# Performance work log

Measured on AMD Instinct MI355X. Metric: run time of the kernel, lower is better.

Reference implementation:

```python
import jax, jax.numpy as jnp
import numpy as np

IN, H, B = 1024, 1024, 8192
EPS = 1e-5

def _ln(x, g, b):
    mu = jnp.mean(x, axis=-1, keepdims=True)
    var = jnp.mean(jnp.square(x - mu), axis=-1, keepdims=True)
    return (x - mu) * jax.lax.rsqrt(var + EPS) * g + b

def setup_inputs() -> dict:
    key = jax.random.key(0)
    ks = jax.random.split(key, 6)
    inp = {
        "input": jax.random.normal(ks[0], (B, IN), dtype=jnp.float32),
        "h_prev": jax.random.normal(ks[1], (B, H), dtype=jnp.float32),
        "c_prev": jax.random.normal(ks[2], (B, H), dtype=jnp.float32),
        # Linear(in, 4H, bias=False) weights, stored [out, in] like torch
        "w_i": jax.random.normal(ks[3], (4 * H, IN), dtype=jnp.float32) / np.sqrt(IN),
        "w_h": jax.random.normal(ks[4], (4 * H, H), dtype=jnp.float32) / np.sqrt(H),
    }
    for name in ("ln_i", "ln_h", "ln_g", "ln_o", "ln_c"):
        inp[name + "_g"] = jnp.ones((H,), dtype=jnp.float32)
        inp[name + "_b"] = jnp.zeros((H,), dtype=jnp.float32)
    return inp

def reference(input, h_prev, c_prev, w_i, w_h,
              ln_i_g, ln_i_b, ln_h_g, ln_h_b, ln_g_g, ln_g_b,
              ln_o_g, ln_o_b, ln_c_g, ln_c_b):
    gi = input @ w_i.T            # [B, 4H]
    gh = h_prev @ w_h.T           # [B, 4H]
    i_i, i_f, i_gc, i_o = jnp.split(gi, 4, axis=-1)
    h_i, h_f, h_g, h_o = jnp.split(gh, 4, axis=-1)
    i_g = jax.nn.sigmoid(_ln(i_i + h_i, ln_i_g, ln_i_b))
    f_g = jax.nn.sigmoid(_ln(i_f + h_f, ln_h_g, ln_h_b))
    # NOTE: faithful to source bug — uses sigmoided i_g (not chunk i_gc) here
    g_g = jnp.tanh(_ln(i_g + h_g, ln_g_g, ln_g_b))
    o_g = jax.nn.sigmoid(_ln(i_o + h_o, ln_o_g, ln_o_b))
    c_new = _ln(f_g * c_prev + i_g * g_g, ln_c_g, ln_c_b)
    h_new = o_g * jnp.tanh(c_new)
    return (h_new, c_new)
```

## Files before the change

kernel.cpp:

```cpp
#include <hip/hip_runtime.h>
#include <hip/hip_bf16.h>

#define BATCH 8192
#define HDIM  1024
#define KDIM  2048
#define NDIM  4096

__device__ inline unsigned short f2bf(float x) {
    unsigned int u = __float_as_uint(x);
    unsigned int r = (u + 0x7fffu + ((u >> 16) & 1u)) >> 16;
    return (unsigned short)r;
}

__global__ __launch_bounds__(256) void convert_w_kernel(
    const float* __restrict__ wi, const float* __restrict__ wh,
    unsigned short* __restrict__ Wb)
{
    int idx = blockIdx.x * 256 + threadIdx.x;
    int n = idx >> 9;
    int k = (idx & 511) << 2;
    float4 v;
    if (k < 1024) {
        if (n >= 2048 && n < 3072) {
            v = make_float4(0.f, 0.f, 0.f, 0.f);
        } else {
            v = *(const float4*)(wi + (size_t)n * 1024 + k);
        }
    } else {
        v = *(const float4*)(wh + (size_t)n * 1024 + (k - 1024));
    }
    ushort4 o;
    o.x = f2bf(v.x); o.y = f2bf(v.y); o.z = f2bf(v.z); o.w = f2bf(v.w);
    *(ushort4*)(Wb + (size_t)n * KDIM + k) = o;
}

__global__ __launch_bounds__(256) void convert_x_kernel(
    const float* __restrict__ input, const float* __restrict__ h_prev,
    unsigned short* __restrict__ Xb)
{
    int idx = blockIdx.x * 256 + threadIdx.x;
    int r = idx >> 9;
    int k = (idx & 511) << 2;
    float4 v;
    if (k < 1024) {
        v = *(const float4*)(input + (size_t)r * 1024 + k);
    } else {
        v = *(const float4*)(h_prev + (size_t)r * 1024 + (k - 1024));
    }
    ushort4 o;
    o.x = f2bf(v.x); o.y = f2bf(v.y); o.z = f2bf(v.z); o.w = f2bf(v.w);
    *(ushort4*)(Xb + (size_t)r * KDIM + k) = o;
}

#define BM 256
#define BN 128
#define BK 64

typedef __attribute__((ext_vector_type(8))) short bf16x8;
typedef __attribute__((ext_vector_type(4))) float f32x4;

__global__ __launch_bounds__(512) void gemm_bt_kernel(
    const unsigned short* __restrict__ A,
    const unsigned short* __restrict__ Bw,
    float* __restrict__ C,
    int M)
{
    __shared__ unsigned short As[BM * BK];
    __shared__ unsigned short Bs[BN * BK];

    const int tid  = threadIdx.x;
    const int lane = tid & 63;
    const int wave = tid >> 6;

    const int bid = blockIdx.x;
    const int bm  = (bid >> 5) * BM;
    const int bn  = (bid & 31) * BN;

    f32x4 acc[4][4] = {};

    const int wm = (wave >> 1) * 64;
    const int wn = (wave & 1) * 64;

    const int srow = lane >> 3;
    const int c_sw = (lane & 7) ^ srow;

    int k0 = 0;
    if (bn >= 2048 && bn < 3072) k0 = 1024;

    for (; k0 < KDIM; k0 += BK) {
#pragma unroll
        for (int p = 0; p < 4; ++p) {
            const int rbase = wave * 32 + p * 8;
            const unsigned short* gA =
                A + (size_t)(bm + rbase + srow) * KDIM + k0 + c_sw * 8;
            __builtin_amdgcn_global_load_lds(
                (const __attribute__((address_space(1))) void*)gA,
                (__attribute__((address_space(3))) void*)&As[rbase * BK], 16, 0, 0);
        }
#pragma unroll
        for (int p = 0; p < 2; ++p) {
            const int rbase = wave * 16 + p * 8;
            const unsigned short* gB =
                Bw + (size_t)(bn + rbase + srow) * KDIM + k0 + c_sw * 8;
            __builtin_amdgcn_global_load_lds(
                (const __attribute__((address_space(1))) void*)gB,
                (__attribute__((address_space(3))) void*)&Bs[rbase * BK], 16, 0, 0);
        }
        __syncthreads();

#pragma unroll
        for (int kk = 0; kk < 2; ++kk) {
            bf16x8 af[4], bfr[4];
            const int cbase = kk * 4 + (lane >> 4);
#pragma unroll
            for (int i = 0; i < 4; ++i) {
                const int ra = wm + i * 16 + (lane & 15);
                af[i]  = *(const bf16x8*)&As[ra * BK + ((cbase ^ (ra & 7)) * 8)];
                const int rb = wn + i * 16 + (lane & 15);
                bfr[i] = *(const bf16x8*)&Bs[rb * BK + ((cbase ^ (rb & 7)) * 8)];
            }
#pragma unroll
            for (int i = 0; i < 4; ++i)
#pragma unroll
                for (int j = 0; j < 4; ++j)
                    acc[i][j] = __builtin_amdgcn_mfma_f32_16x16x32_bf16(
                        af[i], bfr[j], acc[i][j], 0, 0, 0);
        }
        __syncthreads();
    }

#pragma unroll
    for (int i = 0; i < 4; ++i) {
#pragma unroll
        for (int j = 0; j < 4; ++j) {
#pragma unroll
            for (int r = 0; r < 4; ++r) {
                int row = bm + wm + i * 16 + (lane >> 4) * 4 + r;
                int col = bn + wn + j * 16 + (lane & 15);
                C[(size_t)row * NDIM + col] = acc[i][j][r];
            }
        }
    }
}

__device__ inline float sigmoid_f(float x) { return 1.f / (1.f + __expf(-x)); }
__device__ inline float tanh_f(float x) { return 1.f - 2.f / (__expf(2.f * x) + 1.f); }

__device__ inline void wstats(const float* x, float& mu, float& rs)
{
    float s = 0.f, q = 0.f;
#pragma unroll
    for (int e = 0; e < 16; ++e) { s += x[e]; q += x[e] * x[e]; }
#pragma unroll
    for (int o = 1; o < 64; o <<= 1) {
        s += __shfl_xor(s, o);
        q += __shfl_xor(q, o);
    }
    mu = s * (1.f / 1024.f);
    float var = q * (1.f / 1024.f) - mu * mu;
    rs = rsqrtf(var + 1e-5f);
}

#define LOAD16(dst, base)                                              \
    _Pragma("unroll")                                                  \
    for (int j = 0; j < 4; ++j) {                                      \
        float4 t = *(const float4*)((base) + j * 256 + cbase);         \
        dst[4 * j] = t.x; dst[4 * j + 1] = t.y;                        \
        dst[4 * j + 2] = t.z; dst[4 * j + 3] = t.w;                    \
    }

__global__ __launch_bounds__(256) void lstm_ew_kernel(
    const float* __restrict__ G,
    const float* __restrict__ c_prev,
    const float* __restrict__ p0g, const float* __restrict__ p0b,
    const float* __restrict__ p1g, const float* __restrict__ p1b,
    const float* __restrict__ p2g, const float* __restrict__ p2b,
    const float* __restrict__ p3g, const float* __restrict__ p3b,
    const float* __restrict__ p4g, const float* __restrict__ p4b,
    float* __restrict__ out_h, float* __restrict__ out_c,
    int row_base)
{
    const int lane  = threadIdx.x & 63;
    const int wave  = threadIdx.x >> 6;
    const int r     = blockIdx.x * 4 + wave;
    const int grow  = row_base + r;
    const int cbase = lane * 4;

    const float* Grow = G + (size_t)r * NDIM;

    float tmp[16], pg[16], pb[16];
    float ig[16], cm[16], og[16];
    float mu, rs;

    LOAD16(tmp, Grow);
    wstats(tmp, mu, rs);
    LOAD16(pg, p0g); LOAD16(pb, p0b);
#pragma unroll
    for (int e = 0; e < 16; ++e)
        ig[e] = sigmoid_f((tmp[e] - mu) * rs * pg[e] + pb[e]);

    LOAD16(tmp, Grow + 1024);
    wstats(tmp, mu, rs);
    LOAD16(pg, p1g); LOAD16(pb, p1b);
    LOAD16(cm, c_prev + (size_t)grow * HDIM);
#pragma unroll
    for (int e = 0; e < 16; ++e)
        cm[e] *= sigmoid_f((tmp[e] - mu) * rs * pg[e] + pb[e]);

    LOAD16(tmp, Grow + 2048);
#pragma unroll
    for (int e = 0; e < 16; ++e) tmp[e] += ig[e];
    wstats(tmp, mu, rs);
    LOAD16(pg, p2g); LOAD16(pb, p2b);
#pragma unroll
    for (int e = 0; e < 16; ++e)
        cm[e] += ig[e] * tanh_f((tmp[e] - mu) * rs * pg[e] + pb[e]);

    LOAD16(tmp, Grow + 3072);
    wstats(tmp, mu, rs);
    LOAD16(pg, p3g); LOAD16(pb, p3b);
#pragma unroll
    for (int e = 0; e < 16; ++e)
        og[e] = sigmoid_f((tmp[e] - mu) * rs * pg[e] + pb[e]);

    wstats(cm, mu, rs);
    LOAD16(pg, p4g); LOAD16(pb, p4b);
    float cn[16], hn[16];
#pragma unroll
    for (int e = 0; e < 16; ++e) {
        cn[e] = (cm[e] - mu) * rs * pg[e] + pb[e];
        hn[e] = og[e] * tanh_f(cn[e]);
    }

    float* oh = out_h + (size_t)grow * HDIM;
    float* oc = out_c + (size_t)grow * HDIM;
#pragma unroll
    for (int j = 0; j < 4; ++j) {
        *(float4*)(oh + j * 256 + cbase) =
            make_float4(hn[4 * j], hn[4 * j + 1], hn[4 * j + 2], hn[4 * j + 3]);
        *(float4*)(oc + j * 256 + cbase) =
            make_float4(cn[4 * j], cn[4 * j + 1], cn[4 * j + 2], cn[4 * j + 3]);
    }
}

extern "C" void kernel_launch(void* const* d_in, const int* in_sizes, int n_in,
                              void* d_out, int out_size, void* d_ws, size_t ws_size,
                              hipStream_t stream)
{
    const float* input  = (const float*)d_in[0];
    const float* h_prev = (const float*)d_in[1];
    const float* c_prev = (const float*)d_in[2];
    const float* w_i    = (const float*)d_in[3];
    const float* w_h    = (const float*)d_in[4];
    const float* lng[10];
    for (int i = 0; i < 10; ++i) lng[i] = (const float*)d_in[5 + i];

    unsigned short* Xb = (unsigned short*)d_ws;
    size_t xb_bytes = (size_t)BATCH * KDIM * 2;
    unsigned short* Wb = (unsigned short*)((char*)d_ws + xb_bytes);
    size_t wb_bytes = (size_t)NDIM * KDIM * 2;
    float* G = (float*)((char*)d_ws + xb_bytes + wb_bytes);

    size_t g_avail = (ws_size > xb_bytes + wb_bytes) ? (ws_size - xb_bytes - wb_bytes) : 0;
    long max_rows = (long)(g_avail / ((size_t)NDIM * sizeof(float)));
    int chunk = (max_rows >= BATCH) ? BATCH : (int)((max_rows / BM) * BM);
    if (chunk <= 0) chunk = BM;

    convert_w_kernel<<<(NDIM * 512) / 256, 256, 0, stream>>>(w_i, w_h, Wb);
    convert_x_kernel<<<(BATCH * 512) / 256, 256, 0, stream>>>(input, h_prev, Xb);

    float* out_h = (float*)d_out;
    float* out_c = out_h + (size_t)BATCH * HDIM;

    for (int rb = 0; rb < BATCH; rb += chunk) {
        int rows = (BATCH - rb < chunk) ? (BATCH - rb) : chunk;
        gemm_bt_kernel<<<(rows / BM) * (NDIM / BN), 512, 0, stream>>>(
            Xb + (size_t)rb * KDIM, Wb, G, rows);
        lstm_ew_kernel<<<rows / 4, 256, 0, stream>>>(
            G, c_prev, lng[0], lng[1], lng[2], lng[3], lng[4],
            lng[5], lng[6], lng[7], lng[8], lng[9], out_h, out_c, rb);
    }
}
```

Measured before the change: 353.0 us.

## Store GEMM gate outputs as bf16 and merge conversion kernels

The GEMM now writes its gate pre-activations as bf16 instead of fp32, which halves the intermediate buffer's write and read traffic between the GEMM and the elementwise LSTM kernel. The elementwise kernel reads eight bf16 values per lane with wide loads and adjusts its fp32 load and store indexing to match. The two weight and activation conversion kernels are merged into a single launch. Rounding the gates to bf16 before layernorm adds precision error, and the smaller intermediate may let larger chunks fit in the workspace.

```diff
diff --git a/kernel.cpp b/kernel.cpp
--- a/kernel.cpp
+++ b/kernel.cpp
@@ -11,45 +11,40 @@
     unsigned int r = (u + 0x7fffu + ((u >> 16) & 1u)) >> 16;
     return (unsigned short)r;
 }
-
-__global__ __launch_bounds__(256) void convert_w_kernel(
+__device__ inline float bf2f(unsigned short u) {
+    return __uint_as_float((unsigned int)u << 16);
+}
+
+__global__ __launch_bounds__(256) void convert_kernel(
     const float* __restrict__ wi, const float* __restrict__ wh,
-    unsigned short* __restrict__ Wb)
+    const float* __restrict__ input, const float* __restrict__ h_prev,
+    unsigned short* __restrict__ Wb, unsigned short* __restrict__ Xb)
 {
     int idx = blockIdx.x * 256 + threadIdx.x;
-    int n = idx >> 9;
-    int k = (idx & 511) << 2;
+    const int NW = NDIM * 512;
     float4 v;
-    if (k < 1024) {
-        if (n >= 2048 && n < 3072) {
-            v = make_float4(0.f, 0.f, 0.f, 0.f);
+    unsigned short* dst;
+    if (idx < NW) {
+        int n = idx >> 9;
+        int k = (idx & 511) << 2;
+        if (k < 1024) {
+            if (n >= 2048 && n < 3072) v = make_float4(0.f, 0.f, 0.f, 0.f);
+            else                       v = *(const float4*)(wi + (size_t)n * 1024 + k);
         } else {
-            v = *(const float4*)(wi + (size_t)n * 1024 + k);
-        }
+            v = *(const float4*)(wh + (size_t)n * 1024 + (k - 1024));
+        }
+        dst = Wb + (size_t)n * KDIM + k;
     } else {
-        v = *(const float4*)(wh + (size_t)n * 1024 + (k - 1024));
+        int j = idx - NW;
+        int r = j >> 9;
+        int k = (j & 511) << 2;
+        if (k < 1024) v = *(const float4*)(input  + (size_t)r * 1024 + k);
+        else          v = *(const float4*)(h_prev + (size_t)r * 1024 + (k - 1024));
+        dst = Xb + (size_t)r * KDIM + k;
     }
     ushort4 o;
     o.x = f2bf(v.x); o.y = f2bf(v.y); o.z = f2bf(v.z); o.w = f2bf(v.w);
-    *(ushort4*)(Wb + (size_t)n * KDIM + k) = o;
-}
-
-__global__ __launch_bounds__(256) void convert_x_kernel(
-    const float* __restrict__ input, const float* __restrict__ h_prev,
-    unsigned short* __restrict__ Xb)
-{
-    int idx = blockIdx.x * 256 + threadIdx.x;
-    int r = idx >> 9;
-    int k = (idx & 511) << 2;
-    float4 v;
-    if (k < 1024) {
-        v = *(const float4*)(input + (size_t)r * 1024 + k);
-    } else {
-        v = *(const float4*)(h_prev + (size_t)r * 1024 + (k - 1024));
-    }
-    ushort4 o;
-    o.x = f2bf(v.x); o.y = f2bf(v.y); o.z = f2bf(v.z); o.w = f2bf(v.w);
-    *(ushort4*)(Xb + (size_t)r * KDIM + k) = o;
+    *(ushort4*)dst = o;
 }
 
 #define BM 256
@@ -62,7 +57,7 @@
 __global__ __launch_bounds__(512) void gemm_bt_kernel(
     const unsigned short* __restrict__ A,
     const unsigned short* __restrict__ Bw,
-    float* __restrict__ C,
+    unsigned short* __restrict__ G,
     int M)
 {
     __shared__ unsigned short As[BM * BK];
@@ -137,7 +132,7 @@
             for (int r = 0; r < 4; ++r) {
                 int row = bm + wm + i * 16 + (lane >> 4) * 4 + r;
                 int col = bn + wn + j * 16 + (lane & 15);
-                C[(size_t)row * NDIM + col] = acc[i][j][r];
+                G[(size_t)row * NDIM + col] = f2bf(acc[i][j][r]);
             }
         }
     }
@@ -145,6 +140,8 @@
 
 __device__ inline float sigmoid_f(float x) { return 1.f / (1.f + __expf(-x)); }
 __device__ inline float tanh_f(float x) { return 1.f - 2.f / (__expf(2.f * x) + 1.f); }
+
+typedef __attribute__((ext_vector_type(8))) unsigned short us8;
 
 __device__ inline void wstats(const float* x, float& mu, float& rs)
 {
@@ -161,16 +158,27 @@
     rs = rsqrtf(var + 1e-5f);
 }
 
-#define LOAD16(dst, base)                                              \
+#define LOADG16(dst, basep)                                            \
     _Pragma("unroll")                                                  \
-    for (int j = 0; j < 4; ++j) {                                      \
-        float4 t = *(const float4*)((base) + j * 256 + cbase);         \
-        dst[4 * j] = t.x; dst[4 * j + 1] = t.y;                        \
-        dst[4 * j + 2] = t.z; dst[4 * j + 3] = t.w;                    \
+    for (int j = 0; j < 2; ++j) {                                      \
+        us8 t = *(const us8*)((basep) + j * 512 + cbase);              \
+        _Pragma("unroll")                                              \
+        for (int e = 0; e < 8; ++e) dst[j * 8 + e] = bf2f(t[e]);       \
+    }
+
+#define LOADF16(dst, basep)                                            \
+    _Pragma("unroll")                                                  \
+    for (int j = 0; j < 2; ++j) {                                      \
+        float4 a = *(const float4*)((basep) + j * 512 + cbase);        \
+        float4 b = *(const float4*)((basep) + j * 512 + cbase + 4);    \
+        dst[j * 8 + 0] = a.x; dst[j * 8 + 1] = a.y;                    \
+        dst[j * 8 + 2] = a.z; dst[j * 8 + 3] = a.w;                    \
+        dst[j * 8 + 4] = b.x; dst[j * 8 + 5] = b.y;                    \
+        dst[j * 8 + 6] = b.z; dst[j * 8 + 7] = b.w;                    \
     }
 
 __global__ __launch_bounds__(256) void lstm_ew_kernel(
-    const float* __restrict__ G,
+    const unsigned short* __restrict__ G,
     const float* __restrict__ c_prev,
     const float* __restrict__ p0g, const float* __restrict__ p0b,
     const float* __restrict__ p1g, const float* __restrict__ p1b,
@@ -184,47 +192,47 @@
     const int wave  = threadIdx.x >> 6;
     const int r     = blockIdx.x * 4 + wave;
     const int grow  = row_base + r;
-    const int cbase = lane * 4;
-
-    const float* Grow = G + (size_t)r * NDIM;
+    const int cbase = lane * 8;
+
+    const unsigned short* Grow = G + (size_t)r * NDIM;
 
     float tmp[16], pg[16], pb[16];
     float ig[16], cm[16], og[16];
     float mu, rs;
 
-    LOAD16(tmp, Grow);
-    wstats(tmp, mu, rs);
-    LOAD16(pg, p0g); LOAD16(pb, p0b);
+    LOADG16(tmp, Grow);
+    wstats(tmp, mu, rs);
+    LOADF16(pg, p0g); LOADF16(pb, p0b);
 #pragma unroll
     for (int e = 0; e < 16; ++e)
         ig[e] = sigmoid_f((tmp[e] - mu) * rs * pg[e] + pb[e]);
 
-    LOAD16(tmp, Grow + 1024);
-    wstats(tmp, mu, rs);
-    LOAD16(pg, p1g); LOAD16(pb, p1b);
-    LOAD16(cm, c_prev + (size_t)grow * HDIM);
+    LOADG16(tmp, Grow + 1024);
+    wstats(tmp, mu, rs);
+    LOADF16(pg, p1g); LOADF16(pb, p1b);
+    LOADF16(cm, c_prev + (size_t)grow * HDIM);
 #pragma unroll
     for (int e = 0; e < 16; ++e)
         cm[e] *= sigmoid_f((tmp[e] - mu) * rs * pg[e] + pb[e]);
 
-    LOAD16(tmp, Grow + 2048);
+    LOADG16(tmp, Grow + 2048);
 #pragma unroll
     for (int e = 0; e < 16; ++e) tmp[e] += ig[e];
     wstats(tmp, mu, rs);
-    LOAD16(pg, p2g); LOAD16(pb, p2b);
+    LOADF16(pg, p2g); LOADF16(pb, p2b);
 #pragma unroll
     for (int e = 0; e < 16; ++e)
         cm[e] += ig[e] * tanh_f((tmp[e] - mu) * rs * pg[e] + pb[e]);
 
-    LOAD16(tmp, Grow + 3072);
-    wstats(tmp, mu, rs);
-    LOAD16(pg, p3g); LOAD16(pb, p3b);
+    LOADG16(tmp, Grow + 3072);
+    wstats(tmp, mu, rs);
+    LOADF16(pg, p3g); LOADF16(pb, p3b);
 #pragma unroll
     for (int e = 0; e < 16; ++e)
         og[e] = sigmoid_f((tmp[e] - mu) * rs * pg[e] + pb[e]);
 
     wstats(cm, mu, rs);
-    LOAD16(pg, p4g); LOAD16(pb, p4b);
+    LOADF16(pg, p4g); LOADF16(pb, p4b);
     float cn[16], hn[16];
 #pragma unroll
     for (int e = 0; e < 16; ++e) {
@@ -235,11 +243,15 @@
     float* oh = out_h + (size_t)grow * HDIM;
     float* oc = out_c + (size_t)grow * HDIM;
 #pragma unroll
-    for (int j = 0; j < 4; ++j) {
-        *(float4*)(oh + j * 256 + cbase) =
-            make_float4(hn[4 * j], hn[4 * j + 1], hn[4 * j + 2], hn[4 * j + 3]);
-        *(float4*)(oc + j * 256 + cbase) =
-            make_float4(cn[4 * j], cn[4 * j + 1], cn[4 * j + 2], cn[4 * j + 3]);
+    for (int j = 0; j < 2; ++j) {
+        *(float4*)(oh + j * 512 + cbase) =
+            make_float4(hn[j*8+0], hn[j*8+1], hn[j*8+2], hn[j*8+3]);
+        *(float4*)(oh + j * 512 + cbase + 4) =
+            make_float4(hn[j*8+4], hn[j*8+5], hn[j*8+6], hn[j*8+7]);
+        *(float4*)(oc + j * 512 + cbase) =
+            make_float4(cn[j*8+0], cn[j*8+1], cn[j*8+2], cn[j*8+3]);
+        *(float4*)(oc + j * 512 + cbase + 4) =
+            make_float4(cn[j*8+4], cn[j*8+5], cn[j*8+6], cn[j*8+7]);
     }
 }
 
@@ -259,15 +271,15 @@
     size_t xb_bytes = (size_t)BATCH * KDIM * 2;
     unsigned short* Wb = (unsigned short*)((char*)d_ws + xb_bytes);
     size_t wb_bytes = (size_t)NDIM * KDIM * 2;
-    float* G = (float*)((char*)d_ws + xb_bytes + wb_bytes);
+    unsigned short* G = (unsigned short*)((char*)d_ws + xb_bytes + wb_bytes);
 
     size_t g_avail = (ws_size > xb_bytes + wb_bytes) ? (ws_size - xb_bytes - wb_bytes) : 0;
-    long max_rows = (long)(g_avail / ((size_t)NDIM * sizeof(float)));
+    long max_rows = (long)(g_avail / ((size_t)NDIM * sizeof(unsigned short)));
     int chunk = (max_rows >= BATCH) ? BATCH : (int)((max_rows / BM) * BM);
     if (chunk <= 0) chunk = BM;
 
-    convert_w_kernel<<<(NDIM * 512) / 256, 256, 0, stream>>>(w_i, w_h, Wb);
-    convert_x_kernel<<<(BATCH * 512) / 256, 256, 0, stream>>>(input, h_prev, Xb);
+    convert_kernel<<<(NDIM * 512 + BATCH * 512) / 256, 256, 0, stream>>>(
+        w_i, w_h, input, h_prev, Wb, Xb);
 
     float* out_h = (float*)d_out;
     float* out_c = out_h + (size_t)BATCH * HDIM;
```

New measurement: 335.1 us. 1.05x faster.
